# Kernel tuning notes

Hardware: AMD Instinct MI355X
Metric: run time of the kernel (lower is better)

The kernel has to match this reference:

```python
import jax, jax.numpy as jnp
import numpy as np

B, N, D, H = 8, 1024, 1024, 16
DH = D // H
REL_VOCAB = 6  # stadia + 2
NEG_INF = -1e9


def setup_inputs() -> dict:
    key = jax.random.key(0)
    ks = jax.random.split(key, 8)
    hid = jax.random.normal(ks[0], (B, N, D), dtype=jnp.float32)
    adj = jax.random.randint(ks[1], (B, N, N), 0, 2, dtype=jnp.int32)
    relative_pos = jax.random.randint(ks[2], (B, N, N), 0, REL_VOCAB, dtype=jnp.int32)
    s = 1.0 / np.sqrt(D)
    Wq = jax.random.normal(ks[3], (D, D), dtype=jnp.float32) * s
    Wk = jax.random.normal(ks[4], (D, D), dtype=jnp.float32) * s
    Wv = jax.random.normal(ks[5], (D, D), dtype=jnp.float32) * s
    rel_table = jax.random.normal(ks[6], (REL_VOCAB, 1), dtype=jnp.float32)
    ln_gamma = jnp.ones((D,), dtype=jnp.float32)
    ln_beta = jnp.zeros((D,), dtype=jnp.float32)
    return {"hid": hid, "adj": adj, "relative_pos": relative_pos,
            "Wq": Wq, "Wk": Wk, "Wv": Wv, "rel_table": rel_table,
            "ln_gamma": ln_gamma, "ln_beta": ln_beta}


def _layer_norm(x, gamma, beta, eps=1e-5):
    mu = jnp.mean(x, axis=-1, keepdims=True)
    var = jnp.var(x, axis=-1, keepdims=True)
    return (x - mu) * jax.lax.rsqrt(var + eps) * gamma + beta


def reference(hid, adj, relative_pos, Wq, Wk, Wv, rel_table, ln_gamma, ln_beta):
    # relative position bias: embedding dim 1, squeezed -> [B, N, N]
    rel_bias = rel_table[relative_pos][..., 0]
    # projections, split into heads: [B, N, H, DH]
    q = (hid @ Wq).reshape(B, N, H, DH)
    k = (hid @ Wk).reshape(B, N, H, DH)
    v = (hid @ Wv).reshape(B, N, H, DH)
    # scores [B, H, N, N], scaled by sqrt(key_dim) = sqrt(D)
    scores = jnp.einsum('bqhd,bkhd->bhqk', q, k) / jnp.sqrt(jnp.float32(D))
    scores = scores + rel_bias[:, None, :, :]
    mask = (adj != 0)[:, None, :, :]
    scores = jnp.where(mask, scores, NEG_INF)
    attn = jax.nn.softmax(scores, axis=-1)
    out = jnp.einsum('bhqk,bkhd->bqhd', attn, v).reshape(B, N, D)
    out = jax.nn.relu(out) + hid  # activation + residual
    return _layer_norm(out, ln_gamma, ln_beta)
```

## Files before the change

### kernel.cpp

```cpp
#include <hip/hip_runtime.h>
#include <math.h>

#define Bc 8
#define Nc 1024
#define Dc 1024
#define Hc 16
#define DHc 64
#define NEGINF -1e9f
#define LOG2E 1.44269504f

typedef unsigned int  u32;
typedef unsigned short u16;
typedef unsigned long long u64;
typedef u16  u16x8 __attribute__((ext_vector_type(8)));
typedef u16  u16x4 __attribute__((ext_vector_type(4)));
typedef u32  u32x2 __attribute__((ext_vector_type(2)));
typedef int  i32x4 __attribute__((ext_vector_type(4)));
typedef __bf16 bf16x8 __attribute__((ext_vector_type(8)));
typedef float f32x4 __attribute__((ext_vector_type(4)));

__device__ __forceinline__ u16 f2bf(float f) {
    u32 u = __builtin_bit_cast(u32, f);
    u += 0x7fffu + ((u >> 16) & 1u);
    return (u16)(u >> 16);
}
__device__ __forceinline__ float bf2f(u16 b) {
    return __builtin_bit_cast(float, (u32)b << 16);
}
__device__ __forceinline__ u32 pack2bf(float lo, float hi) {
    return __builtin_amdgcn_perm(__builtin_bit_cast(u32, hi),
                                 __builtin_bit_cast(u32, lo), 0x07060302u);
}
__device__ __forceinline__ float exp2_raw(float x) {
    float r;
    asm("v_exp_f32 %0, %1" : "=v"(r) : "v"(x));
    return r;
}

__device__ __forceinline__ void glds16(const u16* g, const u16* l) {
    __builtin_amdgcn_global_load_lds(
        (const __attribute__((address_space(1))) void*)(u64)g,
        (__attribute__((address_space(3))) void*)(u32)(u64)l, 16, 0, 0);
}

__global__ __launch_bounds__(256) void prep_fused(
    const int* __restrict__ adj, const int* __restrict__ relpos,
    const float* __restrict__ rel_table, u16* __restrict__ bias,
    const float* __restrict__ hid, u16* __restrict__ hidb,
    const float* __restrict__ Wq, const float* __restrict__ Wk,
    const float* __restrict__ Wv, u16* __restrict__ WqT,
    u16* __restrict__ WkT, u16* __restrict__ WvT)
{
    const int blk = blockIdx.x;
    const int t = threadIdx.x;

    if (blk < 2048) {
        __shared__ u16 tblb[8];
        if (t < 8) {
            float v = (t < 6) ? rel_table[t] * LOG2E : NEGINF;
            tblb[t] = f2bf(v);
        }
        __syncthreads();
        const int gid = blk * 256 + t;
        const int o16 = gid << 4;
        const int row = o16 >> 10;
        const int p0  = o16 & 1023;
        const int blkb = p0 & ~63;
        const int tt  = (p0 >> 4) & 3;
        const size_t base = ((size_t)row << 10) + blkb + 4 * tt;
        i32x4 a4[4], r4[4];
#pragma unroll
        for (int u = 0; u < 4; ++u) {
            a4[u] = *(const i32x4*)&adj[base + 16 * u];
            r4[u] = *(const i32x4*)&relpos[base + 16 * u];
        }
        u16x8 o0, o1;
#pragma unroll
        for (int s = 0; s < 8; ++s) {
            const int u = s & 3, e = s >> 2;
            o0[s] = tblb[a4[u][e] ? r4[u][e] : 6];
        }
#pragma unroll
        for (int s = 8; s < 16; ++s) {
            const int u = s & 3, e = s >> 2;
            o1[s - 8] = tblb[a4[u][e] ? r4[u][e] : 6];
        }
        *(u16x8*)&bias[(size_t)o16]     = o0;
        *(u16x8*)&bias[(size_t)o16 + 8] = o1;
    } else if (blk < 6144) {
        int idx = (blk - 2048) * 256 + t;
        float4 a = ((const float4*)hid)[2 * idx];
        float4 b = ((const float4*)hid)[2 * idx + 1];
        u16x8 o;
        o[0] = f2bf(a.x); o[1] = f2bf(a.y); o[2] = f2bf(a.z); o[3] = f2bf(a.w);
        o[4] = f2bf(b.x); o[5] = f2bf(b.y); o[6] = f2bf(b.z); o[7] = f2bf(b.w);
        ((u16x8*)hidb)[idx] = o;
    } else {
        __shared__ float tile[32][33];
        const int wb = blk - 6144;
        const int x = wb & 31, y = (wb >> 5) & 31, z = wb >> 10;
        const float* W; u16* WT;
        if (z == 0)      { W = Wq; WT = WqT; }
        else if (z == 1) { W = Wk; WT = WkT; }
        else             { W = Wv; WT = WvT; }
        const int tx = t & 31, ty = t >> 5;
        const int n0 = x * 32, k0 = y * 32;
#pragma unroll
        for (int i = 0; i < 4; ++i) {
            int r = ty + i * 8;
            tile[r][tx] = W[(size_t)(k0 + r) * Dc + n0 + tx];
        }
        __syncthreads();
#pragma unroll
        for (int i = 0; i < 4; ++i) {
            int n = ty + i * 8;
            WT[(size_t)(n0 + n) * Dc + k0 + tx] = f2bf(tile[tx][n]);
        }
    }
}

__global__ __launch_bounds__(256) void qkv_mfma(
    const u16* __restrict__ hidb, const u16* __restrict__ WqT,
    const u16* __restrict__ WkT, const u16* __restrict__ WvT,
    u16* __restrict__ qo, u16* __restrict__ ko, u16* __restrict__ vo)
{
    __shared__ u16 As[128 * 64];
    __shared__ u16 Bs[128 * 64];

    const int by = blockIdx.y;
    const int z = by >> 3;
    const int c0 = (by & 7) << 7;
    const int row0 = blockIdx.x << 7;
    const u16* WT; u16* out;
    if (z == 0)      { WT = WqT; out = qo; }
    else if (z == 1) { WT = WkT; out = ko; }
    else             { WT = WvT; out = vo; }
    const float qsc = (z == 0) ? 0.03125f : 1.0f;

    const int tid = threadIdx.x;
    const int wave = tid >> 6, lane = tid & 63;
    const int g = lane >> 4, li = lane & 15;
    const int wr = wave >> 1, wc = wave & 1;
    const int lr = lane >> 3, ls = lane & 7;
    const int sseg = ls ^ lr;

    const u16* pa = hidb + (size_t)(row0 + wave * 32 + lr) * Dc + sseg * 8;
    const u16* pb = WT   + (size_t)(c0   + wave * 32 + lr) * Dc + sseg * 8;
    u16* la = &As[(wave * 32) * 64];
    u16* lb = &Bs[(wave * 32) * 64];

    f32x4 acc[4][4] = {};

    const int swz = (li & 7);

    for (int kt = 0; kt < Dc; kt += 64) {
        __syncthreads();
#pragma unroll
        for (int i = 0; i < 4; ++i) {
            glds16(pa + kt + i * 8 * Dc, la + i * 8 * 64);
            glds16(pb + kt + i * 8 * Dc, lb + i * 8 * 64);
        }
        __syncthreads();
#pragma unroll
        for (int ks = 0; ks < 2; ++ks) {
            const int soff = ((ks * 4 + g) ^ swz) * 8;
            bf16x8 af[4], bf[4];
#pragma unroll
            for (int mi = 0; mi < 4; ++mi)
                af[mi] = *(const bf16x8*)&As[(wr * 64 + mi * 16 + li) * 64 + soff];
#pragma unroll
            for (int nj = 0; nj < 4; ++nj)
                bf[nj] = *(const bf16x8*)&Bs[(wc * 64 + nj * 16 + li) * 64 + soff];
#pragma unroll
            for (int mi = 0; mi < 4; ++mi)
#pragma unroll
                for (int nj = 0; nj < 4; ++nj)
                    acc[mi][nj] = __builtin_amdgcn_mfma_f32_16x16x32_bf16(
                        af[mi], bf[nj], acc[mi][nj], 0, 0, 0);
        }
    }

    const int b = row0 >> 10;

    if (z != 2) {
        const int h2 = (c0 + wc * 64) >> 6;
        const int nbase = (row0 & 1023) + wr * 64 + g * 4;
#pragma unroll
        for (int mi = 0; mi < 4; ++mi)
#pragma unroll
            for (int rr = 0; rr < 4; ++rr) {
                int n = nbase + mi * 16 + rr;
                u32x2 pk;
                pk.x = (u32)f2bf(acc[mi][0][rr] * qsc) | ((u32)f2bf(acc[mi][1][rr] * qsc) << 16);
                pk.y = (u32)f2bf(acc[mi][2][rr] * qsc) | ((u32)f2bf(acc[mi][3][rr] * qsc) << 16);
                *(u32x2*)(out + ((size_t)(b * Hc + h2) * Nc + n) * DHc + 4 * li) = pk;
            }
    } else {
        __syncthreads();
        u16* T = ((wave & 2) ? Bs : As) + (wave & 1) * 4096;
#pragma unroll
        for (int mi = 0; mi < 4; ++mi)
#pragma unroll
            for (int rr = 0; rr < 4; ++rr) {
                int r = mi * 16 + g * 4 + rr;
                int pp = ((r & 15) << 2) | (r >> 4);
#pragma unroll
                for (int nj = 0; nj < 4; ++nj) {
                    int c = nj * 16 + li;
                    T[c * 64 + ((((pp >> 3) ^ (c & 7)) << 3) | (pp & 7))]
                        = f2bf(acc[mi][nj][rr]);
                }
            }
        const int nseg = ls ^ lr;
#pragma unroll
        for (int i = 0; i < 8; ++i) {
            int cl = i * 8 + lr;
            u16x8 val = *(const u16x8*)&T[cl * 64 + ls * 8];
            int cz = c0 + wc * 64 + cl;
            int n = (row0 & 1023) + wr * 64 + nseg * 8;
            *(u16x8*)&vo[(((size_t)(b * Hc + (cz >> 6)) * DHc + (cz & 63)) * Nc) + n] = val;
        }
    }
}

__global__ __launch_bounds__(256, 3) void attn_mfma(
    const u16* __restrict__ q, const u16* __restrict__ k,
    const u16* __restrict__ v, const u16* __restrict__ bias,
    float* __restrict__ attn_out)
{
    __shared__ u16 Ks[2][64 * 64];
    __shared__ u16 VTs[2][64 * 64];
    __shared__ u16 PQ[128 * 64];

    const int tid = threadIdx.x;
    const int w = tid >> 6, lane = tid & 63;
    const int g = lane >> 4, li = lane & 15;
    const int lr8 = lane >> 3, ls8 = lane & 7;
    const int lseg = ls8 ^ lr8;

    const int id = blockIdx.x;
    const int b  = id & 7;
    const int r_ = id >> 3;
    const int h  = r_ & 15;
    const int qt = r_ >> 4;
    const int q0 = qt << 7;

    const u16* kbase = k + (size_t)(b * Hc + h) * Nc * DHc;
    const u16* vbase = v + (size_t)(b * Hc + h) * DHc * Nc;
    const u16* brow  = bias + ((size_t)(b * Nc) + q0 + w * 32) * Nc + 4 * li;

    {
        const u16* kp = kbase + (size_t)(w * 16 + lr8) * DHc + lseg * 8;
        const u16* vp = vbase + (size_t)(w * 16 + lr8) * Nc + lseg * 8;
        glds16(kp,           &Ks[0][(w * 16) * 64]);
        glds16(kp + 8 * DHc, &Ks[0][(w * 16) * 64 + 8 * 64]);
        glds16(vp,           &VTs[0][(w * 16) * 64]);
        glds16(vp + 8 * Nc,  &VTs[0][(w * 16) * 64 + 8 * 64]);
    }

    {
        const int sr = tid >> 1;
        const int sh = (tid & 1) * 32;
        const int sw = (sr & 7) << 3;
        const u16* qp = q + ((size_t)((b * Hc + h) * Nc) + q0 + sr) * DHc + sh;
        u16* dst = &PQ[sr * 64];
        *(u16x8*)(dst + ((sh +  0) ^ sw)) = *(const u16x8*)(qp);
        *(u16x8*)(dst + ((sh +  8) ^ sw)) = *(const u16x8*)(qp + 8);
        *(u16x8*)(dst + ((sh + 16) ^ sw)) = *(const u16x8*)(qp + 16);
        *(u16x8*)(dst + ((sh + 24) ^ sw)) = *(const u16x8*)(qp + 24);
    }

    u16x4 brv[2][4];
#pragma unroll
    for (int mt = 0; mt < 2; ++mt)
#pragma unroll
        for (int r = 0; r < 4; ++r)
            brv[mt][r] = *(const u16x4*)&brow[(size_t)(mt * 16 + g * 4 + r) * Nc];

    bf16x8 qf[2][2];
#pragma unroll
    for (int mt = 0; mt < 2; ++mt)
#pragma unroll
        for (int ks = 0; ks < 2; ++ks)
            qf[mt][ks] = *(const bf16x8*)&PQ[(w * 32 + mt * 16 + li) * 64
                                            + ((ks * 32 + g * 8) ^ ((li & 7) << 3))];

    f32x4 o_[2][4] = {};
    float lsum[2][4] = {};

    for (int it = 0; it < 16; ++it) {
        const int cur = it & 1;
        __syncthreads();

        u16x4 brn[2][4];
        if (it < 15) {
            const int k1 = (it + 1) * 64;
            const u16* kp = kbase + (size_t)(k1 + w * 16 + lr8) * DHc + lseg * 8;
            const u16* vp = vbase + (size_t)(w * 16 + lr8) * Nc + k1 + lseg * 8;
            u16* kl = &Ks[cur ^ 1][(w * 16) * 64];
            u16* vl = &VTs[cur ^ 1][(w * 16) * 64];
            glds16(kp,           kl);
            glds16(kp + 8 * DHc, kl + 8 * 64);
            glds16(vp,           vl);
            glds16(vp + 8 * Nc,  vl + 8 * 64);
#pragma unroll
            for (int mt = 0; mt < 2; ++mt)
#pragma unroll
                for (int r = 0; r < 4; ++r)
                    brn[mt][r] = *(const u16x4*)&brow[(size_t)(mt * 16 + g * 4 + r) * Nc + k1];
        }

        f32x4 sacc[2][4] = {};
        __builtin_amdgcn_s_setprio(1);
#pragma unroll
        for (int ks = 0; ks < 2; ++ks) {
            const int so = (((ks << 2) | g) ^ (li & 7)) << 3;
#pragma unroll
            for (int nt = 0; nt < 4; ++nt) {
                bf16x8 kf = *(const bf16x8*)&Ks[cur][(nt * 16 + li) * 64 + so];
                sacc[0][nt] = __builtin_amdgcn_mfma_f32_16x16x32_bf16(qf[0][ks], kf, sacc[0][nt], 0, 0, 0);
                sacc[1][nt] = __builtin_amdgcn_mfma_f32_16x16x32_bf16(qf[1][ks], kf, sacc[1][nt], 0, 0, 0);
            }
        }
        __builtin_amdgcn_s_setprio(0);

#pragma unroll
        for (int mt = 0; mt < 2; ++mt)
#pragma unroll
            for (int r = 0; r < 4; ++r) {
                const int qrl = w * 32 + mt * 16 + g * 4 + r;
                float pv[4];
#pragma unroll
                for (int nt = 0; nt < 4; ++nt) {
                    pv[nt] = exp2_raw(fmaf(sacc[mt][nt][r], LOG2E,
                                           bf2f(brv[mt][r][nt])));
                    lsum[mt][r] += pv[nt];
                }
                u32* dst = (u32*)&PQ[(qrl & ~7) * 64
                                     + (((qrl & 7) * 64 + li * 4) ^ ((qrl & 7) << 3))];
                dst[0] = pack2bf(pv[0], pv[1]);
                dst[1] = pack2bf(pv[2], pv[3]);
            }

        __builtin_amdgcn_s_setprio(1);
#pragma unroll
        for (int ks = 0; ks < 2; ++ks) {
            const int so = (((ks << 2) | g) ^ (li & 7)) << 3;
            const int po = (ks * 32 + g * 8) ^ ((li & 7) << 3);
            bf16x8 pa0 = *(const bf16x8*)&PQ[(w * 32 + li) * 64 + po];
            bf16x8 pa1 = *(const bf16x8*)&PQ[(w * 32 + 16 + li) * 64 + po];
#pragma unroll
            for (int j = 0; j < 4; ++j) {
                bf16x8 vf = *(const bf16x8*)&VTs[cur][(j * 16 + li) * 64 + so];
                o_[0][j] = __builtin_amdgcn_mfma_f32_16x16x32_bf16(pa0, vf, o_[0][j], 0, 0, 0);
                o_[1][j] = __builtin_amdgcn_mfma_f32_16x16x32_bf16(pa1, vf, o_[1][j], 0, 0, 0);
            }
        }
        __builtin_amdgcn_s_setprio(0);

        if (it < 15) {
#pragma unroll
            for (int mt = 0; mt < 2; ++mt)
#pragma unroll
                for (int r = 0; r < 4; ++r)
                    brv[mt][r] = brn[mt][r];
        }
    }

#pragma unroll
    for (int mt = 0; mt < 2; ++mt)
#pragma unroll
        for (int r = 0; r < 4; ++r) {
            float l = lsum[mt][r];
            l += __shfl_xor(l, 1);
            l += __shfl_xor(l, 2);
            l += __shfl_xor(l, 4);
            l += __shfl_xor(l, 8);
            float inv = 1.f / l;
            int qrow = q0 + w * 32 + mt * 16 + g * 4 + r;
            float* op = attn_out + ((size_t)b * Nc + qrow) * Dc + h * DHc;
#pragma unroll
            for (int j = 0; j < 4; ++j)
                op[j * 16 + li] = o_[mt][j][r] * inv;
        }
}

__global__ __launch_bounds__(256) void ln_kernel(
    const float* attn_out, const float* __restrict__ hid,
    const float* __restrict__ gamma, const float* __restrict__ beta,
    float* out)
{
    const int row  = blockIdx.x * 4 + (threadIdx.x >> 6);
    const int lane = threadIdx.x & 63;
    const float* ap = attn_out + (size_t)row * Dc;
    const float* hp = hid + (size_t)row * Dc;

    float4 x[4];
    float s1 = 0.f, s2 = 0.f;
#pragma unroll
    for (int j = 0; j < 4; ++j) {
        const int c = 4 * (lane + 64 * j);
        float4 a = *(const float4*)&ap[c];
        float4 h = *(const float4*)&hp[c];
        x[j].x = fmaxf(a.x, 0.f) + h.x;
        x[j].y = fmaxf(a.y, 0.f) + h.y;
        x[j].z = fmaxf(a.z, 0.f) + h.z;
        x[j].w = fmaxf(a.w, 0.f) + h.w;
        s1 += x[j].x + x[j].y + x[j].z + x[j].w;
        s2 += x[j].x * x[j].x + x[j].y * x[j].y
            + x[j].z * x[j].z + x[j].w * x[j].w;
    }
#pragma unroll
    for (int off = 1; off < 64; off <<= 1) {
        s1 += __shfl_xor(s1, off);
        s2 += __shfl_xor(s2, off);
    }

    float mu  = s1 * (1.f / 1024.f);
    float var = s2 * (1.f / 1024.f) - mu * mu;
    float rstd = rsqrtf(var + 1e-5f);

#pragma unroll
    for (int j = 0; j < 4; ++j) {
        const int c = 4 * (lane + 64 * j);
        float4 g  = *(const float4*)&gamma[c];
        float4 be = *(const float4*)&beta[c];
        float4 r4;
        r4.x = (x[j].x - mu) * rstd * g.x + be.x;
        r4.y = (x[j].y - mu) * rstd * g.y + be.y;
        r4.z = (x[j].z - mu) * rstd * g.z + be.z;
        r4.w = (x[j].w - mu) * rstd * g.w + be.w;
        *(float4*)&out[(size_t)row * Dc + c] = r4;
    }
}

extern "C" void kernel_launch(void* const* d_in, const int* in_sizes, int n_in,
                              void* d_out, int out_size, void* d_ws, size_t ws_size,
                              hipStream_t stream) {
    const float* hid       = (const float*)d_in[0];
    const int*   adj       = (const int*)d_in[1];
    const int*   relpos    = (const int*)d_in[2];
    const float* Wq        = (const float*)d_in[3];
    const float* Wk        = (const float*)d_in[4];
    const float* Wv        = (const float*)d_in[5];
    const float* rel_table = (const float*)d_in[6];
    const float* gamma     = (const float*)d_in[7];
    const float* beta      = (const float*)d_in[8];
    float* out = (float*)d_out;

    const size_t per  = (size_t)Bc * Hc * Nc * DHc;
    const size_t wsz  = (size_t)Dc * Dc;
    u16* qb   = (u16*)d_ws;
    u16* kb   = qb + per;
    u16* vb   = kb + per;
    u16* bias = vb + per;
    u16* hidb = bias + (size_t)Bc * Nc * Nc;
    u16* wqT  = hidb + (size_t)Bc * Nc * Dc;
    u16* wkT  = wqT + wsz;
    u16* wvT  = wkT + wsz;

    prep_fused<<<9216, 256, 0, stream>>>(adj, relpos, rel_table, bias,
                                         hid, hidb, Wq, Wk, Wv, wqT, wkT, wvT);
    qkv_mfma<<<dim3(64, 24), 256, 0, stream>>>(hidb, wqT, wkT, wvT, qb, kb, vb);
    attn_mfma<<<1024, 256, 0, stream>>>(qb, kb, vb, bias, out);
    ln_kernel<<<2048, 256, 0, stream>>>(out, hid, gamma, beta, out);
}
```

Baseline: 275.5 us.

## Move bias-table construction into QKV GEMM launch to overlap with MFMA work

The adj/relpos-to-bias conversion moves out of the prep kernel and into extra blocks of the QKV projection kernel. The grid's y dimension grows from 24 to 56, with 3 of every 7 y-slices running the GEMM and 4 doing bias work. The goal is to let the memory-bound bias pass run alongside the compute-bound GEMM rather than before it. In exchange, bias blocks share the GEMM's LDS allocation, which can reduce occupancy, and the interleaved block scheduling may disturb GEMM cache reuse.

New measurement: 279.1 us. Within noise of the previous version (+1.3%).

```diff
diff --git a/kernel.cpp b/kernel.cpp
--- a/kernel.cpp
+++ b/kernel.cpp
@@ -43,9 +43,7 @@
         (__attribute__((address_space(3))) void*)(u32)(u64)l, 16, 0, 0);
 }
 
-__global__ __launch_bounds__(256) void prep_fused(
-    const int* __restrict__ adj, const int* __restrict__ relpos,
-    const float* __restrict__ rel_table, u16* __restrict__ bias,
+__global__ __launch_bounds__(256) void prep1(
     const float* __restrict__ hid, u16* __restrict__ hidb,
     const float* __restrict__ Wq, const float* __restrict__ Wk,
     const float* __restrict__ Wv, u16* __restrict__ WqT,
@@ -54,41 +52,8 @@
     const int blk = blockIdx.x;
     const int t = threadIdx.x;
 
-    if (blk < 2048) {
-        __shared__ u16 tblb[8];
-        if (t < 8) {
-            float v = (t < 6) ? rel_table[t] * LOG2E : NEGINF;
-            tblb[t] = f2bf(v);
-        }
-        __syncthreads();
-        const int gid = blk * 256 + t;
-        const int o16 = gid << 4;
-        const int row = o16 >> 10;
-        const int p0  = o16 & 1023;
-        const int blkb = p0 & ~63;
-        const int tt  = (p0 >> 4) & 3;
-        const size_t base = ((size_t)row << 10) + blkb + 4 * tt;
-        i32x4 a4[4], r4[4];
-#pragma unroll
-        for (int u = 0; u < 4; ++u) {
-            a4[u] = *(const i32x4*)&adj[base + 16 * u];
-            r4[u] = *(const i32x4*)&relpos[base + 16 * u];
-        }
-        u16x8 o0, o1;
-#pragma unroll
-        for (int s = 0; s < 8; ++s) {
-            const int u = s & 3, e = s >> 2;
-            o0[s] = tblb[a4[u][e] ? r4[u][e] : 6];
-        }
-#pragma unroll
-        for (int s = 8; s < 16; ++s) {
-            const int u = s & 3, e = s >> 2;
-            o1[s - 8] = tblb[a4[u][e] ? r4[u][e] : 6];
-        }
-        *(u16x8*)&bias[(size_t)o16]     = o0;
-        *(u16x8*)&bias[(size_t)o16 + 8] = o1;
-    } else if (blk < 6144) {
-        int idx = (blk - 2048) * 256 + t;
+    if (blk < 4096) {
+        int idx = blk * 256 + t;
         float4 a = ((const float4*)hid)[2 * idx];
         float4 b = ((const float4*)hid)[2 * idx + 1];
         u16x8 o;
@@ -97,7 +62,7 @@
         ((u16x8*)hidb)[idx] = o;
     } else {
         __shared__ float tile[32][33];
-        const int wb = blk - 6144;
+        const int wb = blk - 4096;
         const int x = wb & 31, y = (wb >> 5) & 31, z = wb >> 10;
         const float* W; u16* WT;
         if (z == 0)      { W = Wq; WT = WqT; }
@@ -119,15 +84,57 @@
     }
 }
 
-__global__ __launch_bounds__(256) void qkv_mfma(
+__global__ __launch_bounds__(256) void qkv_bias_mfma(
     const u16* __restrict__ hidb, const u16* __restrict__ WqT,
     const u16* __restrict__ WkT, const u16* __restrict__ WvT,
-    u16* __restrict__ qo, u16* __restrict__ ko, u16* __restrict__ vo)
+    u16* __restrict__ qo, u16* __restrict__ ko, u16* __restrict__ vo,
+    const int* __restrict__ adj, const int* __restrict__ relpos,
+    const float* __restrict__ rel_table, u16* __restrict__ bias)
 {
     __shared__ u16 As[128 * 64];
     __shared__ u16 Bs[128 * 64];
 
-    const int by = blockIdx.y;
+    const int t = threadIdx.x;
+    const int ym = blockIdx.y % 7;
+    const int yg = blockIdx.y / 7;
+
+    if (ym >= 3) {
+        const int bid = (yg * 4 + (ym - 3)) * 64 + blockIdx.x;
+        if (t < 8) {
+            float v = (t < 6) ? rel_table[t] * LOG2E : NEGINF;
+            As[t] = f2bf(v);
+        }
+        __syncthreads();
+        const int gid = bid * 256 + t;
+        const int o16 = gid << 4;
+        const int row = o16 >> 10;
+        const int p0  = o16 & 1023;
+        const int blkb = p0 & ~63;
+        const int tt  = (p0 >> 4) & 3;
+        const size_t base = ((size_t)row << 10) + blkb + 4 * tt;
+        i32x4 a4[4], r4[4];
+#pragma unroll
+        for (int u = 0; u < 4; ++u) {
+            a4[u] = *(const i32x4*)&adj[base + 16 * u];
+            r4[u] = *(const i32x4*)&relpos[base + 16 * u];
+        }
+        u16x8 o0, o1;
+#pragma unroll
+        for (int s = 0; s < 8; ++s) {
+            const int u = s & 3, e = s >> 2;
+            o0[s] = As[a4[u][e] ? r4[u][e] : 6];
+        }
+#pragma unroll
+        for (int s = 8; s < 16; ++s) {
+            const int u = s & 3, e = s >> 2;
+            o1[s - 8] = As[a4[u][e] ? r4[u][e] : 6];
+        }
+        *(u16x8*)&bias[(size_t)o16]     = o0;
+        *(u16x8*)&bias[(size_t)o16 + 8] = o1;
+        return;
+    }
+
+    const int by = yg * 3 + ym;
     const int z = by >> 3;
     const int c0 = (by & 7) << 7;
     const int row0 = blockIdx.x << 7;
@@ -137,7 +144,7 @@
     else             { WT = WvT; out = vo; }
     const float qsc = (z == 0) ? 0.03125f : 1.0f;
 
-    const int tid = threadIdx.x;
+    const int tid = t;
     const int wave = tid >> 6, lane = tid & 63;
     const int g = lane >> 4, li = lane & 15;
     const int wr = wave >> 1, wc = wave & 1;
@@ -459,9 +466,9 @@
     u16* wkT  = wqT + wsz;
     u16* wvT  = wkT + wsz;
 
-    prep_fused<<<9216, 256, 0, stream>>>(adj, relpos, rel_table, bias,
-                                         hid, hidb, Wq, Wk, Wv, wqT, wkT, wvT);
-    qkv_mfma<<<dim3(64, 24), 256, 0, stream>>>(hidb, wqT, wkT, wvT, qb, kb, vb);
+    prep1<<<7168, 256, 0, stream>>>(hid, hidb, Wq, Wk, Wv, wqT, wkT, wvT);
+    qkv_bias_mfma<<<dim3(64, 56), 256, 0, stream>>>(
+        hidb, wqT, wkT, wvT, qb, kb, vb, adj, relpos, rel_table, bias);
     attn_mfma<<<1024, 256, 0, stream>>>(qb, kb, vb, bias, out);
     ln_kernel<<<2048, 256, 0, stream>>>(out, hid, gamma, beta, out);
 }
```

## Process two 128-row query tiles per attention block to reuse K/V tiles

Applied to the files above, without the earlier changes.

Each attention block now handles 256 query rows (two 128-row sub-tiles) against the same staged K and V tiles, halving the grid to 512 blocks and halving K/V global-to-LDS traffic per query row. Q fragments are loaded straight from global memory into registers instead of through LDS. Bias loads are no longer prefetched one iteration ahead but issued at the top of each iteration. Accumulator and Q registers double, so launch bounds drop to 2 blocks per SM, which together with the halved grid reduces parallelism and latency hiding.

Result: no change. 280.4 us (+1.8%).

```diff
diff --git a/kernel.cpp b/kernel.cpp
--- a/kernel.cpp
+++ b/kernel.cpp
@@ -223,7 +223,7 @@
     }
 }
 
-__global__ __launch_bounds__(256, 3) void attn_mfma(
+__global__ __launch_bounds__(256, 2) void attn_mfma(
     const u16* __restrict__ q, const u16* __restrict__ k,
     const u16* __restrict__ v, const u16* __restrict__ bias,
     float* __restrict__ attn_out)
@@ -242,8 +242,8 @@
     const int b  = id & 7;
     const int r_ = id >> 3;
     const int h  = r_ & 15;
-    const int qt = r_ >> 4;
-    const int q0 = qt << 7;
+    const int qp = r_ >> 4;
+    const int q0 = qp << 8;
 
     const u16* kbase = k + (size_t)(b * Hc + h) * Nc * DHc;
     const u16* vbase = v + (size_t)(b * Hc + h) * DHc * Nc;
@@ -258,41 +258,24 @@
         glds16(vp + 8 * Nc,  &VTs[0][(w * 16) * 64 + 8 * 64]);
     }
 
-    {
-        const int sr = tid >> 1;
-        const int sh = (tid & 1) * 32;
-        const int sw = (sr & 7) << 3;
-        const u16* qp = q + ((size_t)((b * Hc + h) * Nc) + q0 + sr) * DHc + sh;
-        u16* dst = &PQ[sr * 64];
-        *(u16x8*)(dst + ((sh +  0) ^ sw)) = *(const u16x8*)(qp);
-        *(u16x8*)(dst + ((sh +  8) ^ sw)) = *(const u16x8*)(qp + 8);
-        *(u16x8*)(dst + ((sh + 16) ^ sw)) = *(const u16x8*)(qp + 16);
-        *(u16x8*)(dst + ((sh + 24) ^ sw)) = *(const u16x8*)(qp + 24);
-    }
-
-    u16x4 brv[2][4];
-#pragma unroll
-    for (int mt = 0; mt < 2; ++mt)
-#pragma unroll
-        for (int r = 0; r < 4; ++r)
-            brv[mt][r] = *(const u16x4*)&brow[(size_t)(mt * 16 + g * 4 + r) * Nc];
-
-    bf16x8 qf[2][2];
-#pragma unroll
-    for (int mt = 0; mt < 2; ++mt)
-#pragma unroll
-        for (int ks = 0; ks < 2; ++ks)
-            qf[mt][ks] = *(const bf16x8*)&PQ[(w * 32 + mt * 16 + li) * 64
-                                            + ((ks * 32 + g * 8) ^ ((li & 7) << 3))];
-
-    f32x4 o_[2][4] = {};
-    float lsum[2][4] = {};
+    bf16x8 qf[2][2][2];
+#pragma unroll
+    for (int t = 0; t < 2; ++t)
+#pragma unroll
+        for (int mt = 0; mt < 2; ++mt)
+#pragma unroll
+            for (int ks = 0; ks < 2; ++ks)
+                qf[t][mt][ks] = *(const bf16x8*)(q
+                    + ((size_t)((b * Hc + h) * Nc) + q0 + t * 128 + w * 32
+                       + mt * 16 + li) * DHc + ks * 32 + g * 8);
+
+    f32x4 o_[2][2][4] = {};
+    float lsum[2][2][4] = {};
 
     for (int it = 0; it < 16; ++it) {
         const int cur = it & 1;
         __syncthreads();
 
-        u16x4 brn[2][4];
         if (it < 15) {
             const int k1 = (it + 1) * 64;
             const u16* kp = kbase + (size_t)(k1 + w * 16 + lr8) * DHc + lseg * 8;
@@ -303,86 +286,88 @@
             glds16(kp + 8 * DHc, kl + 8 * 64);
             glds16(vp,           vl);
             glds16(vp + 8 * Nc,  vl + 8 * 64);
+        }
+
+        u16x4 brv[2][2][4];
+#pragma unroll
+        for (int t = 0; t < 2; ++t)
 #pragma unroll
             for (int mt = 0; mt < 2; ++mt)
 #pragma unroll
                 for (int r = 0; r < 4; ++r)
-                    brn[mt][r] = *(const u16x4*)&brow[(size_t)(mt * 16 + g * 4 + r) * Nc + k1];
-        }
-
-        f32x4 sacc[2][4] = {};
-        __builtin_amdgcn_s_setprio(1);
-#pragma unroll
-        for (int ks = 0; ks < 2; ++ks) {
-            const int so = (((ks << 2) | g) ^ (li & 7)) << 3;
-#pragma unroll
-            for (int nt = 0; nt < 4; ++nt) {
-                bf16x8 kf = *(const bf16x8*)&Ks[cur][(nt * 16 + li) * 64 + so];
-                sacc[0][nt] = __builtin_amdgcn_mfma_f32_16x16x32_bf16(qf[0][ks], kf, sacc[0][nt], 0, 0, 0);
-                sacc[1][nt] = __builtin_amdgcn_mfma_f32_16x16x32_bf16(qf[1][ks], kf, sacc[1][nt], 0, 0, 0);
+                    brv[t][mt][r] = *(const u16x4*)&brow[
+                        (size_t)(t * 128 + mt * 16 + g * 4 + r) * Nc + it * 64];
+
+#pragma unroll
+        for (int t = 0; t < 2; ++t) {
+            f32x4 sacc[2][4] = {};
+            __builtin_amdgcn_s_setprio(1);
+#pragma unroll
+            for (int ks = 0; ks < 2; ++ks) {
+                const int so = (((ks << 2) | g) ^ (li & 7)) << 3;
+#pragma unroll
+                for (int nt = 0; nt < 4; ++nt) {
+                    bf16x8 kf = *(const bf16x8*)&Ks[cur][(nt * 16 + li) * 64 + so];
+                    sacc[0][nt] = __builtin_amdgcn_mfma_f32_16x16x32_bf16(qf[t][0][ks], kf, sacc[0][nt], 0, 0, 0);
+                    sacc[1][nt] = __builtin_amdgcn_mfma_f32_16x16x32_bf16(qf[t][1][ks], kf, sacc[1][nt], 0, 0, 0);
+                }
             }
-        }
-        __builtin_amdgcn_s_setprio(0);
-
+            __builtin_amdgcn_s_setprio(0);
+
+#pragma unroll
+            for (int mt = 0; mt < 2; ++mt)
+#pragma unroll
+                for (int r = 0; r < 4; ++r) {
+                    const int qrl = w * 32 + mt * 16 + g * 4 + r;
+                    float pv[4];
+#pragma unroll
+                    for (int nt = 0; nt < 4; ++nt) {
+                        pv[nt] = exp2_raw(fmaf(sacc[mt][nt][r], LOG2E,
+                                               bf2f(brv[t][mt][r][nt])));
+                        lsum[t][mt][r] += pv[nt];
+                    }
+                    u32* dst = (u32*)&PQ[(qrl & ~7) * 64
+                                         + (((qrl & 7) * 64 + li * 4) ^ ((qrl & 7) << 3))];
+                    dst[0] = pack2bf(pv[0], pv[1]);
+                    dst[1] = pack2bf(pv[2], pv[3]);
+                }
+
+            __builtin_amdgcn_s_setprio(1);
+#pragma unroll
+            for (int ks = 0; ks < 2; ++ks) {
+                const int so = (((ks << 2) | g) ^ (li & 7)) << 3;
+                const int po = (ks * 32 + g * 8) ^ ((li & 7) << 3);
+                bf16x8 pa0 = *(const bf16x8*)&PQ[(w * 32 + li) * 64 + po];
+                bf16x8 pa1 = *(const bf16x8*)&PQ[(w * 32 + 16 + li) * 64 + po];
+#pragma unroll
+                for (int j = 0; j < 4; ++j) {
+                    bf16x8 vf = *(const bf16x8*)&VTs[cur][(j * 16 + li) * 64 + so];
+                    o_[t][0][j] = __builtin_amdgcn_mfma_f32_16x16x32_bf16(pa0, vf, o_[t][0][j], 0, 0, 0);
+                    o_[t][1][j] = __builtin_amdgcn_mfma_f32_16x16x32_bf16(pa1, vf, o_[t][1][j], 0, 0, 0);
+                }
+            }
+            __builtin_amdgcn_s_setprio(0);
+        }
+    }
+
+#pragma unroll
+    for (int t = 0; t < 2; ++t)
 #pragma unroll
         for (int mt = 0; mt < 2; ++mt)
 #pragma unroll
             for (int r = 0; r < 4; ++r) {
-                const int qrl = w * 32 + mt * 16 + g * 4 + r;
-                float pv[4];
-#pragma unroll
-                for (int nt = 0; nt < 4; ++nt) {
-                    pv[nt] = exp2_raw(fmaf(sacc[mt][nt][r], LOG2E,
-                                           bf2f(brv[mt][r][nt])));
-                    lsum[mt][r] += pv[nt];
-                }
-                u32* dst = (u32*)&PQ[(qrl & ~7) * 64
-                                     + (((qrl & 7) * 64 + li * 4) ^ ((qrl & 7) << 3))];
-                dst[0] = pack2bf(pv[0], pv[1]);
-                dst[1] = pack2bf(pv[2], pv[3]);
+                float l = lsum[t][mt][r];
+                l += __shfl_xor(l, 1);
+                l += __shfl_xor(l, 2);
+                l += __shfl_xor(l, 4);
+                l += __shfl_xor(l, 8);
+                float inv = 1.f / l;
+                int qrow = q0 + t * 128 + w * 32 + mt * 16 + g * 4 + r;
+                float* op = attn_out + ((size_t)b * Nc + qrow) * Dc + h * DHc;
+#pragma unroll
+                for (int j = 0; j < 4; ++j)
+                    op[j * 16 + li] = o_[t][mt][j][r] * inv;
             }
-
-        __builtin_amdgcn_s_setprio(1);
-#pragma unroll
-        for (int ks = 0; ks < 2; ++ks) {
-            const int so = (((ks << 2) | g) ^ (li & 7)) << 3;
-            const int po = (ks * 32 + g * 8) ^ ((li & 7) << 3);
-            bf16x8 pa0 = *(const bf16x8*)&PQ[(w * 32 + li) * 64 + po];
-            bf16x8 pa1 = *(const bf16x8*)&PQ[(w * 32 + 16 + li) * 64 + po];
-#pragma unroll
-            for (int j = 0; j < 4; ++j) {
-                bf16x8 vf = *(const bf16x8*)&VTs[cur][(j * 16 + li) * 64 + so];
-                o_[0][j] = __builtin_amdgcn_mfma_f32_16x16x32_bf16(pa0, vf, o_[0][j], 0, 0, 0);
-                o_[1][j] = __builtin_amdgcn_mfma_f32_16x16x32_bf16(pa1, vf, o_[1][j], 0, 0, 0);
-            }
-        }
-        __builtin_amdgcn_s_setprio(0);
-
-        if (it < 15) {
-#pragma unroll
-            for (int mt = 0; mt < 2; ++mt)
-#pragma unroll
-                for (int r = 0; r < 4; ++r)
-                    brv[mt][r] = brn[mt][r];
-        }
-    }
-
-#pragma unroll
-    for (int mt = 0; mt < 2; ++mt)
-#pragma unroll
-        for (int r = 0; r < 4; ++r) {
-            float l = lsum[mt][r];
-            l += __shfl_xor(l, 1);
-            l += __shfl_xor(l, 2);
-            l += __shfl_xor(l, 4);
-            l += __shfl_xor(l, 8);
-            float inv = 1.f / l;
-            int qrow = q0 + w * 32 + mt * 16 + g * 4 + r;
-            float* op = attn_out + ((size_t)b * Nc + qrow) * Dc + h * DHc;
-#pragma unroll
-            for (int j = 0; j < 4; ++j)
-                op[j * 16 + li] = o_[mt][j][r] * inv;
-        }
 }
 
 __global__ __launch_bounds__(256) void ln_kernel(
@@ -462,6 +447,6 @@
     prep_fused<<<9216, 256, 0, stream>>>(adj, relpos, rel_table, bias,
                                          hid, hidb, Wq, Wk, Wv, wqT, wkT, wvT);
     qkv_mfma<<<dim3(64, 24), 256, 0, stream>>>(hidb, wqT, wkT, wvT, qb, kb, vb);
-    attn_mfma<<<1024, 256, 0, stream>>>(qb, kb, vb, bias, out);
+    attn_mfma<<<512, 256, 0, stream>>>(qb, kb, vb, bias, out);
     ln_kernel<<<2048, 256, 0, stream>>>(out, hid, gamma, beta, out);
 }
```
